# Kernel tuning notes

Measured on AMD Instinct MI355X. Metric: run time of the kernel, lower is better.

## Reference

```python
import jax, jax.numpy as jnp
import numpy as np

H_BANDWIDTH = 0.5
EPS = 1e-5


def setup_inputs() -> dict:
    key = jax.random.key(0)
    k1, k2 = jax.random.split(key)
    x = jax.random.normal(k1, (4, 256, 64, 64), dtype=jnp.float32)
    y = jax.random.normal(k2, (4, 256, 64, 64), dtype=jnp.float32)
    return {"x": x, "y": y}


def reference(x, y):
    # x, y: (N, C, H, W), H=W=64 so no pooling branch is taken
    N, C, H, W = x.shape
    # mean over batch and spatial dims of y -> per-channel mu, shape (1, C, 1, 1)
    y_mu = jnp.mean(y, axis=(0, 2, 3)).reshape(1, C, 1, 1)
    x_c = x - y_mu
    y_c = y - y_mu
    # L2-normalize over channel dim
    x_n = x_c / jnp.linalg.norm(x_c, axis=1, keepdims=True)
    y_n = y_c / jnp.linalg.norm(y_c, axis=1, keepdims=True)
    x_n = x_n.reshape(N, C, H * W)
    y_n = y_n.reshape(N, C, H * W)
    # cosine similarity: (N, HW, HW)
    cos = jnp.einsum("ncp,ncq->npq", x_n, y_n)
    d = 1.0 - cos
    d_min = jnp.min(d, axis=2, keepdims=True)
    d_tilde = d / (d_min + EPS)
    w = jnp.exp((1.0 - d_tilde) / H_BANDWIDTH)
    cx_ij = w / jnp.sum(w, axis=2, keepdims=True)
    cx = jnp.mean(jnp.max(cx_ij, axis=1), axis=1)  # (N,)
    cx_loss = jnp.mean(-jnp.log(cx + EPS))
    return cx_loss
```

## Files before the change

kernel.cpp:

```cpp
#include <hip/hip_runtime.h>
#include <hip/hip_bf16.h>

typedef short bf16x8 __attribute__((ext_vector_type(8)));
typedef float f32x4 __attribute__((ext_vector_type(4)));

#define NB 4
#define C 256
#define HW 4096
#define NROWS (NB * HW)
#define EPSF 1e-5f

__device__ __forceinline__ unsigned short f2bf(float f) {
    unsigned int u = __float_as_uint(f);
    unsigned int r = u + 0x7fffu + ((u >> 16) & 1u);
    return (unsigned short)(r >> 16);
}
__device__ __forceinline__ float bf2f(unsigned int h) {
    return __uint_as_float(h << 16);
}
__device__ __forceinline__ void unpack8(uint4 u, float* v) {
    unsigned int w0 = u.x, w1 = u.y, w2 = u.z, w3 = u.w;
    v[0] = bf2f(w0 & 0xffffu); v[1] = bf2f(w0 >> 16);
    v[2] = bf2f(w1 & 0xffffu); v[3] = bf2f(w1 >> 16);
    v[4] = bf2f(w2 & 0xffffu); v[5] = bf2f(w2 >> 16);
    v[6] = bf2f(w3 & 0xffffu); v[7] = bf2f(w3 >> 16);
}
__device__ __forceinline__ float waveReduceSum(float v) {
    for (int off = 32; off > 0; off >>= 1) v += __shfl_xor(v, off);
    return v;
}
typedef __attribute__((address_space(1))) const unsigned int glb_cu;
typedef __attribute__((address_space(3))) unsigned int lds_u;
__device__ __forceinline__ void async_copy16(const unsigned short* g, unsigned short* l) {
    __builtin_amdgcn_global_load_lds((glb_cu*)g, (lds_u*)l, 16, 0, 0);
}

__global__ __launch_bounds__(256) void mu_kernel(const float* __restrict__ y,
                                                 float* __restrict__ mu) {
    int c = blockIdx.x;
    int tid = threadIdx.x;
    float s = 0.f;
    const float* base = y + (size_t)c * HW;
    for (int n = 0; n < NB; n++) {
        const float* bn = base + (size_t)n * C * HW;
        for (int i = tid; i < HW; i += 256) s += bn[i];
    }
    s = waveReduceSum(s);
    __shared__ float red[4];
    int lane = tid & 63, wave = tid >> 6;
    if (lane == 0) red[wave] = s;
    __syncthreads();
    if (tid == 0) mu[c] = (red[0] + red[1] + red[2] + red[3]) * (1.0f / 16384.0f);
}

#define TP 32
#define TSTRIDE 257
__global__ __launch_bounds__(256) void prep_kernel(const float* __restrict__ x,
                                                   const float* __restrict__ y,
                                                   const float* __restrict__ mu,
                                                   unsigned short* __restrict__ Xn,
                                                   unsigned short* __restrict__ Yn) {
    __shared__ float smu[C];
    __shared__ float tile[TP * TSTRIDE];
    __shared__ float red[8 * 32];
    __shared__ float invn[TP];
    int tid = threadIdx.x;
    smu[tid] = mu[tid];
    int blk = blockIdx.x;
    int n = blk >> 7;
    int p0 = (blk & 127) * TP;
    int tp = tid & 31, cc = tid >> 5;
    __syncthreads();
    for (int pass = 0; pass < 2; pass++) {
        const float* in = pass ? y : x;
        unsigned short* out = pass ? Yn : Xn;
        const float* base = in + (size_t)n * C * HW + p0 + tp;
        float ssq = 0.f;
        for (int c = cc; c < C; c += 8) {
            float v = base[(size_t)c * HW] - smu[c];
            tile[tp * TSTRIDE + c] = v;
            ssq += v * v;
        }
        red[cc * 32 + tp] = ssq;
        __syncthreads();
        if (tid < 32) {
            float s = 0.f;
            for (int k = 0; k < 8; k++) s += red[k * 32 + tid];
            invn[tid] = rsqrtf(s);
        }
        __syncthreads();
        int c2 = (tid & 127) * 2;
        int pp = tid >> 7;
        for (int p = pp; p < TP; p += 2) {
            float inv = invn[p];
            unsigned short b0 = f2bf(tile[p * TSTRIDE + c2] * inv);
            unsigned short b1 = f2bf(tile[p * TSTRIDE + c2 + 1] * inv);
            unsigned int pack = (unsigned int)b0 | ((unsigned int)b1 << 16);
            ((unsigned int*)out)[(size_t)(n * HW + p0 + p) * (C / 2) + (c2 >> 1)] = pack;
        }
        __syncthreads();
    }
}

#define EPSTRIDE 136
#define STAGE(s, b)                                                            \
    do {                                                                       \
        unsigned short* lA = lds_us + (b) * 16384;                             \
        unsigned short* lB = lds_us + (b) * 16384 + 8192;                      \
        _Pragma("unroll")                                                      \
        for (int t = 0; t < 4; t++) {                                          \
            int slot = t * 256 + tid;                                          \
            int r = slot >> 3, cl = slot & 7;                                  \
            int c = (s) * 8 + (cl ^ (r & 7));                                  \
            async_copy16(Ab + (size_t)r * C + c * 8, lA + slot * 8);           \
        }                                                                      \
        _Pragma("unroll")                                                      \
        for (int t = 0; t < 4; t++) {                                          \
            int slot = t * 256 + tid;                                          \
            int r = slot >> 3, cl = slot & 7;                                  \
            int c = (s) * 8 + (cl ^ (r & 7));                                  \
            async_copy16(Bb + (size_t)r * C + c * 8, lB + slot * 8);           \
        }                                                                      \
    } while (0)

#define COMPUTE(b)                                                             \
    do {                                                                       \
        const unsigned short* lA = lds_us + (b) * 16384;                       \
        const unsigned short* lB = lds_us + (b) * 16384 + 8192;                \
        _Pragma("unroll")                                                      \
        for (int kkl = 0; kkl < 2; kkl++) {                                    \
            int cl4 = kkl * 4 + quad;                                          \
            int clp = cl4 ^ (mrow & 7);                                        \
            bf16x8 af[4], bfr[4];                                              \
            _Pragma("unroll")                                                  \
            for (int i = 0; i < 4; i++) {                                      \
                af[i]  = *(const bf16x8*)(lA + (wm + i * 16 + mrow) * 64 + clp * 8); \
                bfr[i] = *(const bf16x8*)(lB + (wn + i * 16 + mrow) * 64 + clp * 8); \
            }                                                                  \
            _Pragma("unroll")                                                  \
            for (int i = 0; i < 4; i++)                                        \
                _Pragma("unroll")                                              \
                for (int j = 0; j < 4; j++)                                    \
                    acc[i][j] = __builtin_amdgcn_mfma_f32_16x16x32_bf16(af[i], bfr[j], acc[i][j], 0, 0, 0); \
        }                                                                      \
    } while (0)

__global__ __launch_bounds__(256, 2) void gemm_cos(const unsigned short* __restrict__ Xn,
                                                   const unsigned short* __restrict__ Yn,
                                                   unsigned short* __restrict__ Cos) {
    __shared__ unsigned short lds_us[32768];
    int n = blockIdx.z;
    int pBase = blockIdx.y * 128, qBase = blockIdx.x * 128;
    const unsigned short* Ab = Xn + ((size_t)n * HW + pBase) * C;
    const unsigned short* Bb = Yn + ((size_t)n * HW + qBase) * C;
    int tid = threadIdx.x, lane = tid & 63, wave = tid >> 6;
    int wm = (wave >> 1) * 64, wn = (wave & 1) * 64;
    int mrow = lane & 15, quad = lane >> 4;

    f32x4 acc[4][4];
#pragma unroll
    for (int i = 0; i < 4; i++)
#pragma unroll
        for (int j = 0; j < 4; j++) acc[i][j] = (f32x4){0.f, 0.f, 0.f, 0.f};

    STAGE(0, 0);
    __syncthreads();

#pragma unroll
    for (int s = 0; s < 3; s++) {
        STAGE(s + 1, (s + 1) & 1);
        __builtin_amdgcn_sched_barrier(0);
        COMPUTE(s & 1);
        __syncthreads();
    }

    COMPUTE(1);
    __syncthreads();

    unsigned short* epb = lds_us;
    int col = lane & 15, quad4 = quad * 4;
#pragma unroll
    for (int i = 0; i < 4; i++)
#pragma unroll
        for (int j = 0; j < 4; j++)
#pragma unroll
            for (int r = 0; r < 4; r++)
                epb[(wm + i * 16 + quad4 + r) * EPSTRIDE + wn + j * 16 + col] = f2bf(acc[i][j][r]);
    __syncthreads();
    unsigned short* Crow = Cos + (size_t)n * HW * HW;
#pragma unroll
    for (int it = 0; it < 8; it++) {
        int e = it * 2048 + tid * 8;
        int r = e >> 7, cg = e & 127;
        uint4 o = *(const uint4*)(epb + r * EPSTRIDE + cg);
        *(uint4*)(Crow + (size_t)(pBase + r) * HW + qBase + cg) = o;
    }
}

__global__ __launch_bounds__(256, 3) void rowcol(const unsigned short* __restrict__ Cos,
                                                 unsigned short* __restrict__ partial) {
    int n = blockIdx.y, chunk = blockIdx.x;
    int tid = threadIdx.x, lane = tid & 63, wave = tid >> 6;
    const unsigned short* rowbase = Cos + ((size_t)n * HW + chunk * 8) * HW;
    __shared__ float redm[8][4];
    __shared__ float sval[8][4];

    uint4 d[8][2];
#pragma unroll
    for (int r = 0; r < 8; r++) {
        const unsigned short* rp = rowbase + (size_t)r * HW;
        d[r][0] = *(const uint4*)(rp + tid * 8);
        d[r][1] = *(const uint4*)(rp + 2048 + tid * 8);
    }

    float m8[8];
#pragma unroll
    for (int r = 0; r < 8; r++) {
        float v[16];
        unpack8(d[r][0], v); unpack8(d[r][1], v + 8);
        float m = v[0];
#pragma unroll
        for (int k = 1; k < 16; k++) m = fmaxf(m, v[k]);
        m8[r] = m;
    }
#pragma unroll
    for (int off = 32; off > 0; off >>= 1)
#pragma unroll
        for (int r = 0; r < 8; r++) m8[r] = fmaxf(m8[r], __shfl_xor(m8[r], off));
    if (lane == 0)
#pragma unroll
        for (int r = 0; r < 8; r++) redm[r][wave] = m8[r];
    __syncthreads();

    float alpha[8], basec[8];
#pragma unroll
    for (int r = 0; r < 8; r++) {
        float M = fmaxf(fmaxf(redm[r][0], redm[r][1]), fmaxf(redm[r][2], redm[r][3]));
        alpha[r] = 2.0f / ((1.0f - M) + EPSF);
        basec[r] = 2.0f - alpha[r];
    }

    float s8[8];
#pragma unroll
    for (int r = 0; r < 8; r++) {
        float v[16];
        unpack8(d[r][0], v); unpack8(d[r][1], v + 8);
        float s = 0.f;
#pragma unroll
        for (int k = 0; k < 16; k++) s += __expf(fmaf(alpha[r], v[k], basec[r]));
        s8[r] = s;
    }
#pragma unroll
    for (int off = 32; off > 0; off >>= 1)
#pragma unroll
        for (int r = 0; r < 8; r++) s8[r] += __shfl_xor(s8[r], off);
    if (lane == 0)
#pragma unroll
        for (int r = 0; r < 8; r++) sval[r][wave] = s8[r];
    __syncthreads();

    float cmax[16];
#pragma unroll
    for (int k = 0; k < 16; k++) cmax[k] = -1e30f;
#pragma unroll
    for (int r = 0; r < 8; r++) {
        float S = sval[r][0] + sval[r][1] + sval[r][2] + sval[r][3];
        float beta = basec[r] - __logf(S);
        float v[16];
        unpack8(d[r][0], v); unpack8(d[r][1], v + 8);
#pragma unroll
        for (int k = 0; k < 16; k++) cmax[k] = fmaxf(cmax[k], fmaf(alpha[r], v[k], beta));
    }

    unsigned short* outp = partial + ((size_t)(n * 512 + chunk)) * HW;
    uint4 o0, o1;
    o0.x = (unsigned int)f2bf(cmax[0]) | ((unsigned int)f2bf(cmax[1]) << 16);
    o0.y = (unsigned int)f2bf(cmax[2]) | ((unsigned int)f2bf(cmax[3]) << 16);
    o0.z = (unsigned int)f2bf(cmax[4]) | ((unsigned int)f2bf(cmax[5]) << 16);
    o0.w = (unsigned int)f2bf(cmax[6]) | ((unsigned int)f2bf(cmax[7]) << 16);
    o1.x = (unsigned int)f2bf(cmax[8]) | ((unsigned int)f2bf(cmax[9]) << 16);
    o1.y = (unsigned int)f2bf(cmax[10]) | ((unsigned int)f2bf(cmax[11]) << 16);
    o1.z = (unsigned int)f2bf(cmax[12]) | ((unsigned int)f2bf(cmax[13]) << 16);
    o1.w = (unsigned int)f2bf(cmax[14]) | ((unsigned int)f2bf(cmax[15]) << 16);
    *(uint4*)(outp + tid * 8) = o0;
    *(uint4*)(outp + 2048 + tid * 8) = o1;
}

__global__ __launch_bounds__(256) void colmax1(const unsigned short* __restrict__ partial,
                                               float* __restrict__ partial2) {
    int n = blockIdx.z, cg = blockIdx.y;
    int q0 = blockIdx.x * 2048 + threadIdx.x * 8;
    const unsigned short* p = partial + ((size_t)(n * 512 + cg * 32)) * HW + q0;
    float mx[8];
#pragma unroll
    for (int k = 0; k < 8; k++) mx[k] = -1e30f;
    for (int c = 0; c < 32; c++) {
        uint4 u = *(const uint4*)(p + (size_t)c * HW);
        float v[8];
        unpack8(u, v);
#pragma unroll
        for (int k = 0; k < 8; k++) mx[k] = fmaxf(mx[k], v[k]);
    }
    float* o = partial2 + ((size_t)(n * 16 + cg)) * HW + q0;
#pragma unroll
    for (int k = 0; k < 8; k += 4) {
        float4 ov = {mx[k], mx[k + 1], mx[k + 2], mx[k + 3]};
        *(float4*)(o + k) = ov;
    }
}

__global__ __launch_bounds__(1024) void colfinal2(const float* __restrict__ partial2,
                                                  float* __restrict__ cxsum) {
    int n = blockIdx.x;
    int tid = threadIdx.x;
    const float* p = partial2 + (size_t)n * 16 * HW + tid * 4;
    float4 m = {-1e30f, -1e30f, -1e30f, -1e30f};
#pragma unroll
    for (int g = 0; g < 16; g++) {
        float4 v = *(const float4*)(p + (size_t)g * HW);
        m.x = fmaxf(m.x, v.x); m.y = fmaxf(m.y, v.y);
        m.z = fmaxf(m.z, v.z); m.w = fmaxf(m.w, v.w);
    }
    float s = __expf(m.x) + __expf(m.y) + __expf(m.z) + __expf(m.w);
    s = waveReduceSum(s);
    __shared__ float red[16];
    int lane = tid & 63, wave = tid >> 6;
    if (lane == 0) red[wave] = s;
    __syncthreads();
    if (tid == 0) {
        float S = 0.f;
        for (int w = 0; w < 16; w++) S += red[w];
        cxsum[n] = S;
    }
}

__global__ void finalize(const float* __restrict__ cxsum, float* __restrict__ out) {
    if (threadIdx.x == 0 && blockIdx.x == 0) {
        float loss = 0.f;
        for (int n = 0; n < NB; n++) {
            float cx = cxsum[n] * (1.0f / 4096.0f);
            loss += -logf(cx + EPSF);
        }
        out[0] = loss * 0.25f;
    }
}

extern "C" void kernel_launch(void* const* d_in, const int* in_sizes, int n_in,
                              void* d_out, int out_size, void* d_ws, size_t ws_size,
                              hipStream_t stream) {
    const float* x = (const float*)d_in[0];
    const float* y = (const float*)d_in[1];
    float* out = (float*)d_out;
    char* ws = (char*)d_ws;

    float* mu               = (float*)(ws + 0);
    float* cxsum            = (float*)(ws + 1024);
    float* partial2         = (float*)(ws + 65536);
    unsigned short* Xn      = (unsigned short*)(ws + 2097152);
    unsigned short* Yn      = (unsigned short*)(ws + 10485760);
    unsigned short* partial = (unsigned short*)(ws + 2097152);
    unsigned short* Cos     = (unsigned short*)(ws + 18874368);

    mu_kernel<<<C, 256, 0, stream>>>(y, mu);
    prep_kernel<<<NROWS / TP, 256, 0, stream>>>(x, y, mu, Xn, Yn);
    gemm_cos<<<dim3(HW / 128, HW / 128, NB), 256, 0, stream>>>(Xn, Yn, Cos);
    rowcol<<<dim3(512, NB), 256, 0, stream>>>(Cos, partial);
    colmax1<<<dim3(2, 16, NB), 256, 0, stream>>>(partial, partial2);
    colfinal2<<<NB, 1024, 0, stream>>>(partial2, cxsum);
    finalize<<<1, 64, 0, stream>>>(cxsum, out);
}
```

Measured before the change: 200.9 us.

## Fuse column-max, exp-sum and finalize into one kernel with atomic ticket

```diff
diff --git a/kernel.cpp b/kernel.cpp
--- a/kernel.cpp
+++ b/kernel.cpp
@@ -36,9 +36,15 @@
 }
 
 __global__ __launch_bounds__(256) void mu_kernel(const float* __restrict__ y,
-                                                 float* __restrict__ mu) {
+                                                 float* __restrict__ mu,
+                                                 float* __restrict__ cxsum,
+                                                 unsigned int* __restrict__ ticket) {
     int c = blockIdx.x;
     int tid = threadIdx.x;
+    if (c == 0) {
+        if (tid < NB) cxsum[tid] = 0.f;
+        if (tid == NB) *ticket = 0u;
+    }
     float s = 0.f;
     const float* base = y + (size_t)c * HW;
     for (int n = 0; n < NB; n++) {
@@ -286,62 +292,41 @@
     *(uint4*)(outp + 2048 + tid * 8) = o1;
 }
 
-__global__ __launch_bounds__(256) void colmax1(const unsigned short* __restrict__ partial,
-                                               float* __restrict__ partial2) {
-    int n = blockIdx.z, cg = blockIdx.y;
-    int q0 = blockIdx.x * 2048 + threadIdx.x * 8;
-    const unsigned short* p = partial + ((size_t)(n * 512 + cg * 32)) * HW + q0;
-    float mx[8];
-#pragma unroll
-    for (int k = 0; k < 8; k++) mx[k] = -1e30f;
-    for (int c = 0; c < 32; c++) {
-        uint4 u = *(const uint4*)(p + (size_t)c * HW);
-        float v[8];
-        unpack8(u, v);
-#pragma unroll
-        for (int k = 0; k < 8; k++) mx[k] = fmaxf(mx[k], v[k]);
-    }
-    float* o = partial2 + ((size_t)(n * 16 + cg)) * HW + q0;
-#pragma unroll
-    for (int k = 0; k < 8; k += 4) {
-        float4 ov = {mx[k], mx[k + 1], mx[k + 2], mx[k + 3]};
-        *(float4*)(o + k) = ov;
-    }
-}
-
-__global__ __launch_bounds__(1024) void colfinal2(const float* __restrict__ partial2,
-                                                  float* __restrict__ cxsum) {
-    int n = blockIdx.x;
+__global__ __launch_bounds__(256) void colred(const unsigned short* __restrict__ partial,
+                                              float* __restrict__ cxsum,
+                                              unsigned int* __restrict__ ticket,
+                                              float* __restrict__ out) {
+    int n = blockIdx.y, g = blockIdx.x;
     int tid = threadIdx.x;
-    const float* p = partial2 + (size_t)n * 16 * HW + tid * 4;
-    float4 m = {-1e30f, -1e30f, -1e30f, -1e30f};
-#pragma unroll
-    for (int g = 0; g < 16; g++) {
-        float4 v = *(const float4*)(p + (size_t)g * HW);
-        m.x = fmaxf(m.x, v.x); m.y = fmaxf(m.y, v.y);
-        m.z = fmaxf(m.z, v.z); m.w = fmaxf(m.w, v.w);
-    }
-    float s = __expf(m.x) + __expf(m.y) + __expf(m.z) + __expf(m.w);
-    s = waveReduceSum(s);
-    __shared__ float red[16];
-    int lane = tid & 63, wave = tid >> 6;
-    if (lane == 0) red[wave] = s;
-    __syncthreads();
-    if (tid == 0) {
-        float S = 0.f;
-        for (int w = 0; w < 16; w++) S += red[w];
-        cxsum[n] = S;
-    }
-}
-
-__global__ void finalize(const float* __restrict__ cxsum, float* __restrict__ out) {
-    if (threadIdx.x == 0 && blockIdx.x == 0) {
-        float loss = 0.f;
-        for (int n = 0; n < NB; n++) {
-            float cx = cxsum[n] * (1.0f / 4096.0f);
-            loss += -logf(cx + EPSF);
+    int qi = tid & 63, cs = tid >> 6;
+    const unsigned short* p = partial + ((size_t)(n * 512 + cs)) * HW + g * 64 + qi;
+    float m = -1e30f;
+#pragma unroll 8
+    for (int c = cs; c < 512; c += 4) {
+        m = fmaxf(m, bf2f(*p));
+        p += (size_t)4 * HW;
+    }
+    __shared__ float sm[4][64];
+    sm[cs][qi] = m;
+    __syncthreads();
+    if (tid < 64) {
+        float mm = fmaxf(fmaxf(sm[0][qi], sm[1][qi]), fmaxf(sm[2][qi], sm[3][qi]));
+        float s = __expf(mm);
+        s = waveReduceSum(s);
+        if (qi == 0) {
+            atomicAdd(&cxsum[n], s);
+            __threadfence();
+            unsigned int old = atomicAdd(ticket, 1u);
+            if (old == (unsigned int)(64 * NB - 1)) {
+                __threadfence();
+                float loss = 0.f;
+                for (int b = 0; b < NB; b++) {
+                    float csn = atomicAdd(&cxsum[b], 0.0f);
+                    loss += -logf(csn * (1.0f / 4096.0f) + EPSF);
+                }
+                out[0] = loss * 0.25f;
+            }
         }
-        out[0] = loss * 0.25f;
     }
 }
 
@@ -355,17 +340,15 @@
 
     float* mu               = (float*)(ws + 0);
     float* cxsum            = (float*)(ws + 1024);
-    float* partial2         = (float*)(ws + 65536);
+    unsigned int* ticket    = (unsigned int*)(ws + 1040);
     unsigned short* Xn      = (unsigned short*)(ws + 2097152);
     unsigned short* Yn      = (unsigned short*)(ws + 10485760);
     unsigned short* partial = (unsigned short*)(ws + 2097152);
     unsigned short* Cos     = (unsigned short*)(ws + 18874368);
 
-    mu_kernel<<<C, 256, 0, stream>>>(y, mu);
+    mu_kernel<<<C, 256, 0, stream>>>(y, mu, cxsum, ticket);
     prep_kernel<<<NROWS / TP, 256, 0, stream>>>(x, y, mu, Xn, Yn);
     gemm_cos<<<dim3(HW / 128, HW / 128, NB), 256, 0, stream>>>(Xn, Yn, Cos);
     rowcol<<<dim3(512, NB), 256, 0, stream>>>(Cos, partial);
-    colmax1<<<dim3(2, 16, NB), 256, 0, stream>>>(partial, partial2);
-    colfinal2<<<NB, 1024, 0, stream>>>(partial2, cxsum);
-    finalize<<<1, 64, 0, stream>>>(cxsum, out);
-}
+    colred<<<dim3(64, NB), 256, 0, stream>>>(partial, cxsum, ticket, out);
+}
```

Result: no change. 203.3 us (+1.2%).
